# Optimization experiments

Measured on AMD Instinct MI355X. Metric: run time of the kernel, lower is better.

## Reference

```python
import jax, jax.numpy as jnp
import numpy as np

DIM = 16
HID = 32

def setup_inputs() -> dict:
    key = jax.random.key(0)
    ks = jax.random.split(key, 5)
    B, S = 32768, 64
    x = jax.random.normal(ks[0], (B, S, DIM), dtype=jnp.float32)
    # LayerNorm params (torch defaults: weight=1, bias=0)
    ln_w = jnp.ones((DIM,), dtype=jnp.float32)
    ln_b = jnp.zeros((DIM,), dtype=jnp.float32)
    # Linear params, torch-style init scale ~ 1/sqrt(fan_in)
    w1 = jax.random.uniform(ks[1], (HID, DIM), jnp.float32, -1.0, 1.0) / np.sqrt(DIM)
    b1 = jax.random.uniform(ks[2], (HID,), jnp.float32, -1.0, 1.0) / np.sqrt(DIM)
    w2 = jax.random.uniform(ks[3], (DIM, HID), jnp.float32, -1.0, 1.0) / np.sqrt(HID)
    b2 = jax.random.uniform(ks[4], (DIM,), jnp.float32, -1.0, 1.0) / np.sqrt(HID)
    return {"x": x, "ln_w": ln_w, "ln_b": ln_b, "w1": w1, "b1": b1, "w2": w2, "b2": b2}

def _layernorm(x, w, b, eps=1e-5):
    mu = jnp.mean(x, axis=-1, keepdims=True)
    var = jnp.mean(jnp.square(x - mu), axis=-1, keepdims=True)
    return (x - mu) * jax.lax.rsqrt(var + eps) * w + b

def reference(x, ln_w, ln_b, w1, b1, w2, b2):
    h = _layernorm(x, ln_w, ln_b)
    h = jnp.einsum('bsd,hd->bsh', h, w1) + b1
    h = jax.nn.gelu(h, approximate=False)  # torch nn.GELU default is exact erf
    h = jnp.einsum('bsh,dh->bsd', h, w2) + b2
    return x + h
```

## Files before the change

### kernel.cpp

```cpp
#include <hip/hip_runtime.h>
#include <math.h>

#define DIM 16
#define HID 32

typedef float v2f __attribute__((ext_vector_type(2)));

__device__ inline float gelu_erf(float x) {
    const float kInvSqrt2 = 0.70710678118654752f;
    float z  = x * kInvSqrt2;
    float az = fabsf(z);
    float t  = __builtin_amdgcn_rcpf(fmaf(0.3275911f, az, 1.0f));
    float e  = __expf(-az * az);
    float p  = fmaf(t, 1.061405429f, -1.453152027f);
    p = fmaf(t, p, 1.421413741f);
    p = fmaf(t, p, -0.284496736f);
    p = fmaf(t, p, 0.254829592f);
    p = p * t;
    float erf_abs = fmaf(-p, e, 1.0f);
    float erfv = copysignf(erf_abs, z);
    return 0.5f * x * (1.0f + erfv);
}

__global__ __launch_bounds__(256) void fused_ln_mlp_kernel(
    const float* __restrict__ x,
    const float* __restrict__ ln_w,
    const float* __restrict__ ln_b,
    const float* __restrict__ w1,
    const float* __restrict__ b1,
    const float* __restrict__ w2,
    const float* __restrict__ b2,
    float* __restrict__ out,
    int nrows)
{
    int row = blockIdx.x * blockDim.x + threadIdx.x;
    if (row >= nrows) return;

    const float* xr = x + (size_t)row * DIM;

    v2f xv2[8];
    {
        float4 t0 = *(const float4*)(xr + 0);
        float4 t1 = *(const float4*)(xr + 4);
        float4 t2 = *(const float4*)(xr + 8);
        float4 t3 = *(const float4*)(xr + 12);
        xv2[0] = (v2f){t0.x, t0.y}; xv2[1] = (v2f){t0.z, t0.w};
        xv2[2] = (v2f){t1.x, t1.y}; xv2[3] = (v2f){t1.z, t1.w};
        xv2[4] = (v2f){t2.x, t2.y}; xv2[5] = (v2f){t2.z, t2.w};
        xv2[6] = (v2f){t3.x, t3.y}; xv2[7] = (v2f){t3.z, t3.w};
    }

    v2f s = xv2[0] + xv2[1];
    s += xv2[2] + xv2[3];
    s += xv2[4] + xv2[5];
    s += xv2[6] + xv2[7];
    float mu = (s.x + s.y) * (1.0f / DIM);

    v2f mu2 = (v2f){mu, mu};
    v2f vs = (v2f){0.0f, 0.0f};
    #pragma unroll
    for (int i = 0; i < 8; i++) {
        v2f d = xv2[i] - mu2;
        vs = __builtin_elementwise_fma(d, d, vs);
    }
    float var = (vs.x + vs.y) * (1.0f / DIM);
    float a = __builtin_amdgcn_rsqf(var + 1e-5f);
    float c = -mu * a;

    const v2f* lnw2 = (const v2f*)ln_w;
    const v2f* lnb2 = (const v2f*)ln_b;
    v2f a2 = (v2f){a, a};
    v2f c2 = (v2f){c, c};
    v2f xn2[8];
    #pragma unroll
    for (int i = 0; i < 8; i++) {
        v2f xhat = __builtin_elementwise_fma(xv2[i], a2, c2);
        xn2[i] = __builtin_elementwise_fma(xhat, lnw2[i], lnb2[i]);
    }

    float g[HID];
    #pragma unroll
    for (int h = 0; h < HID; h++) {
        const v2f* wr = (const v2f*)(w1 + h * DIM);
        v2f acc = (v2f){0.0f, 0.0f};
        #pragma unroll
        for (int j = 0; j < 8; j++) acc = __builtin_elementwise_fma(xn2[j], wr[j], acc);
        float hv = acc.x + acc.y + b1[h];
        g[h] = gelu_erf(hv);
    }

    v2f g2[HID / 2];
    #pragma unroll
    for (int k = 0; k < HID / 2; k++) g2[k] = (v2f){g[2 * k], g[2 * k + 1]};

    float yv[DIM];
    #pragma unroll
    for (int d = 0; d < DIM; d++) {
        const v2f* wr = (const v2f*)(w2 + d * HID);
        v2f acc = (v2f){0.0f, 0.0f};
        #pragma unroll
        for (int k = 0; k < HID / 2; k++) acc = __builtin_elementwise_fma(g2[k], wr[k], acc);
        float xval = (d & 1) ? xv2[d >> 1].y : xv2[d >> 1].x;
        yv[d] = acc.x + acc.y + b2[d] + xval;
    }

    float* outr = out + (size_t)row * DIM;
    *(float4*)(outr + 0)  = make_float4(yv[0],  yv[1],  yv[2],  yv[3]);
    *(float4*)(outr + 4)  = make_float4(yv[4],  yv[5],  yv[6],  yv[7]);
    *(float4*)(outr + 8)  = make_float4(yv[8],  yv[9],  yv[10], yv[11]);
    *(float4*)(outr + 12) = make_float4(yv[12], yv[13], yv[14], yv[15]);
}

extern "C" void kernel_launch(void* const* d_in, const int* in_sizes, int n_in,
                              void* d_out, int out_size, void* d_ws, size_t ws_size,
                              hipStream_t stream) {
    const float* x    = (const float*)d_in[0];
    const float* ln_w = (const float*)d_in[1];
    const float* ln_b = (const float*)d_in[2];
    const float* w1   = (const float*)d_in[3];
    const float* b1   = (const float*)d_in[4];
    const float* w2   = (const float*)d_in[5];
    const float* b2   = (const float*)d_in[6];
    float* out = (float*)d_out;

    int nrows = in_sizes[0] / DIM;
    int block = 256;
    int grid = (nrows + block - 1) / block;

    fused_ln_mlp_kernel<<<grid, block, 0, stream>>>(
        x, ln_w, ln_b, w1, b1, w2, b2, out, nrows);
}
```

Before: 258.3 us.

## Compute both MLP matmuls with bf16 MFMA via per-wave LDS staging

Replaces the per-thread scalar FMA matmuls with bf16 MFMA 16x16x32 instructions. Each wave stages its layernormed rows and the GELU outputs through LDS in bf16 and uses MFMA for both the 16->32 and 32->16 projections. The aim is to cut the VALU cost of the two small matmuls. In exchange it adds bf16 rounding error, LDS traffic, uncoalesced scalar output stores and a second read of x for the residual, and it drops the nrows bounds check.

```diff
diff --git a/kernel.cpp b/kernel.cpp
--- a/kernel.cpp
+++ b/kernel.cpp
@@ -4,7 +4,21 @@
 #define DIM 16
 #define HID 32
 
-typedef float v2f __attribute__((ext_vector_type(2)));
+typedef float  f32x4  __attribute__((ext_vector_type(4)));
+typedef short  bf16x8 __attribute__((ext_vector_type(8)));
+typedef float  v2f    __attribute__((ext_vector_type(2)));
+
+#define ROW_STRIDE_B 80
+#define LDS_PER_WAVE (64 * ROW_STRIDE_B)
+
+__device__ inline unsigned short f2bf(float f) {
+    union { float f; unsigned u; } v; v.f = f;
+    unsigned r = v.u + 0x7fffu + ((v.u >> 16) & 1u);
+    return (unsigned short)(r >> 16);
+}
+__device__ inline unsigned packbf(float lo, float hi) {
+    return (unsigned)f2bf(lo) | ((unsigned)f2bf(hi) << 16);
+}
 
 __device__ inline float gelu_erf(float x) {
     const float kInvSqrt2 = 0.70710678118654752f;
@@ -22,7 +36,7 @@
     return 0.5f * x * (1.0f + erfv);
 }
 
-__global__ __launch_bounds__(256) void fused_ln_mlp_kernel(
+__global__ __launch_bounds__(256) void fused_ln_mlp_mfma(
     const float* __restrict__ x,
     const float* __restrict__ ln_w,
     const float* __restrict__ ln_b,
@@ -33,11 +47,41 @@
     float* __restrict__ out,
     int nrows)
 {
-    int row = blockIdx.x * blockDim.x + threadIdx.x;
-    if (row >= nrows) return;
-
-    const float* xr = x + (size_t)row * DIM;
-
+    __shared__ __align__(16) unsigned char lds_all[4 * LDS_PER_WAVE];
+
+    const int tid  = threadIdx.x;
+    const int lane = tid & 63;
+    const int wave = tid >> 6;
+    const int q    = lane >> 4;
+    const int c    = lane & 15;
+
+    unsigned char* nbuf = lds_all + wave * LDS_PER_WAVE;
+    const int rowbase = (blockIdx.x * 4 + wave) * 64;
+
+    bf16x8 bW1[2];
+    #pragma unroll
+    for (int t = 0; t < 2; t++) {
+        bf16x8 f = {0, 0, 0, 0, 0, 0, 0, 0};
+        if (q < 2) {
+            const float* wp = w1 + (c + 16 * t) * DIM + q * 8;
+            #pragma unroll
+            for (int j = 0; j < 8; j++)
+                ((unsigned short*)&f)[j] = f2bf(wp[j]);
+        }
+        bW1[t] = f;
+    }
+    bf16x8 bW2;
+    {
+        const float* wp = w2 + c * HID + q * 8;
+        #pragma unroll
+        for (int j = 0; j < 8; j++)
+            ((unsigned short*)&bW2)[j] = f2bf(wp[j]);
+    }
+    const float b1v0 = b1[c];
+    const float b1v1 = b1[c + 16];
+    const float b2v  = b2[c];
+
+    const float* xr = x + (size_t)(rowbase + lane) * DIM;
     v2f xv2[8];
     {
         float4 t0 = *(const float4*)(xr + 0);
@@ -49,13 +93,11 @@
         xv2[4] = (v2f){t2.x, t2.y}; xv2[5] = (v2f){t2.z, t2.w};
         xv2[6] = (v2f){t3.x, t3.y}; xv2[7] = (v2f){t3.z, t3.w};
     }
-
     v2f s = xv2[0] + xv2[1];
     s += xv2[2] + xv2[3];
     s += xv2[4] + xv2[5];
     s += xv2[6] + xv2[7];
     float mu = (s.x + s.y) * (1.0f / DIM);
-
     v2f mu2 = (v2f){mu, mu};
     v2f vs = (v2f){0.0f, 0.0f};
     #pragma unroll
@@ -65,50 +107,78 @@
     }
     float var = (vs.x + vs.y) * (1.0f / DIM);
     float a = __builtin_amdgcn_rsqf(var + 1e-5f);
-    float c = -mu * a;
+    float cc = -mu * a;
 
     const v2f* lnw2 = (const v2f*)ln_w;
     const v2f* lnb2 = (const v2f*)ln_b;
     v2f a2 = (v2f){a, a};
-    v2f c2 = (v2f){c, c};
-    v2f xn2[8];
+    v2f c2 = (v2f){cc, cc};
+    float xn[16];
     #pragma unroll
     for (int i = 0; i < 8; i++) {
-        v2f xhat = __builtin_elementwise_fma(xv2[i], a2, c2);
-        xn2[i] = __builtin_elementwise_fma(xhat, lnw2[i], lnb2[i]);
-    }
-
-    float g[HID];
-    #pragma unroll
-    for (int h = 0; h < HID; h++) {
-        const v2f* wr = (const v2f*)(w1 + h * DIM);
-        v2f acc = (v2f){0.0f, 0.0f};
+        v2f xh = __builtin_elementwise_fma(xv2[i], a2, c2);
+        v2f r  = __builtin_elementwise_fma(xh, lnw2[i], lnb2[i]);
+        xn[2 * i]     = r.x;
+        xn[2 * i + 1] = r.y;
+    }
+
+    {
+        int4 w0, w1v, zz;
+        w0.x  = packbf(xn[0],  xn[1]);  w0.y  = packbf(xn[2],  xn[3]);
+        w0.z  = packbf(xn[4],  xn[5]);  w0.w  = packbf(xn[6],  xn[7]);
+        w1v.x = packbf(xn[8],  xn[9]);  w1v.y = packbf(xn[10], xn[11]);
+        w1v.z = packbf(xn[12], xn[13]); w1v.w = packbf(xn[14], xn[15]);
+        zz.x = zz.y = zz.z = zz.w = 0;
+        int4* rowp = (int4*)(nbuf + lane * ROW_STRIDE_B);
+        rowp[0] = w0; rowp[1] = w1v; rowp[2] = zz; rowp[3] = zz;
+    }
+    asm volatile("s_waitcnt lgkmcnt(0)" ::: "memory");
+
+    f32x4 accH[4][2];
+    #pragma unroll
+    for (int rc = 0; rc < 4; rc++) {
+        const bf16x8 afrag =
+            *(const bf16x8*)(nbuf + (rc * 16 + c) * ROW_STRIDE_B + q * 16);
+        f32x4 z0 = {0.f, 0.f, 0.f, 0.f};
+        f32x4 z1 = {0.f, 0.f, 0.f, 0.f};
+        accH[rc][0] = __builtin_amdgcn_mfma_f32_16x16x32_bf16(afrag, bW1[0], z0, 0, 0, 0);
+        accH[rc][1] = __builtin_amdgcn_mfma_f32_16x16x32_bf16(afrag, bW1[1], z1, 0, 0, 0);
+    }
+    asm volatile("s_waitcnt lgkmcnt(0)" ::: "memory");
+
+    #pragma unroll
+    for (int rc = 0; rc < 4; rc++) {
         #pragma unroll
-        for (int j = 0; j < 8; j++) acc = __builtin_elementwise_fma(xn2[j], wr[j], acc);
-        float hv = acc.x + acc.y + b1[h];
-        g[h] = gelu_erf(hv);
-    }
-
-    v2f g2[HID / 2];
-    #pragma unroll
-    for (int k = 0; k < HID / 2; k++) g2[k] = (v2f){g[2 * k], g[2 * k + 1]};
-
-    float yv[DIM];
-    #pragma unroll
-    for (int d = 0; d < DIM; d++) {
-        const v2f* wr = (const v2f*)(w2 + d * HID);
-        v2f acc = (v2f){0.0f, 0.0f};
+        for (int t = 0; t < 2; t++) {
+            #pragma unroll
+            for (int r = 0; r < 4; r++) {
+                float hv = accH[rc][t][r] + (t ? b1v1 : b1v0);
+                float g  = gelu_erf(hv);
+                *(unsigned short*)(nbuf + (rc * 16 + 4 * q + r) * ROW_STRIDE_B
+                                        + (c + 16 * t) * 2) = f2bf(g);
+            }
+        }
+    }
+    asm volatile("s_waitcnt lgkmcnt(0)" ::: "memory");
+
+    f32x4 accY[4];
+    #pragma unroll
+    for (int rc = 0; rc < 4; rc++) {
+        const bf16x8 afrag =
+            *(const bf16x8*)(nbuf + (rc * 16 + c) * ROW_STRIDE_B + q * 16);
+        f32x4 z = {0.f, 0.f, 0.f, 0.f};
+        accY[rc] = __builtin_amdgcn_mfma_f32_16x16x32_bf16(afrag, bW2, z, 0, 0, 0);
+    }
+
+    #pragma unroll
+    for (int rc = 0; rc < 4; rc++) {
         #pragma unroll
-        for (int k = 0; k < HID / 2; k++) acc = __builtin_elementwise_fma(g2[k], wr[k], acc);
-        float xval = (d & 1) ? xv2[d >> 1].y : xv2[d >> 1].x;
-        yv[d] = acc.x + acc.y + b2[d] + xval;
-    }
-
-    float* outr = out + (size_t)row * DIM;
-    *(float4*)(outr + 0)  = make_float4(yv[0],  yv[1],  yv[2],  yv[3]);
-    *(float4*)(outr + 4)  = make_float4(yv[4],  yv[5],  yv[6],  yv[7]);
-    *(float4*)(outr + 8)  = make_float4(yv[8],  yv[9],  yv[10], yv[11]);
-    *(float4*)(outr + 12) = make_float4(yv[12], yv[13], yv[14], yv[15]);
+        for (int r = 0; r < 4; r++) {
+            int grow = rowbase + rc * 16 + 4 * q + r;
+            float xres = x[(size_t)grow * DIM + c];
+            out[(size_t)grow * DIM + c] = accY[rc][r] + b2v + xres;
+        }
+    }
 }
 
 extern "C" void kernel_launch(void* const* d_in, const int* in_sizes, int n_in,
@@ -124,9 +194,9 @@
     float* out = (float*)d_out;
 
     int nrows = in_sizes[0] / DIM;
-    int block = 256;
-    int grid = (nrows + block - 1) / block;
-
-    fused_ln_mlp_kernel<<<grid, block, 0, stream>>>(
+    int rows_per_block = 256;
+    int grid = (nrows + rows_per_block - 1) / rows_per_block;
+
+    fused_ln_mlp_mfma<<<grid, 256, 0, stream>>>(
         x, ln_w, ln_b, w1, b1, w2, b2, out, nrows);
 }
```

Result: no change. 255.0 us (-1.3%).
